# Kernel optimization log

Measured on AMD Instinct MI355X. Metric: run time of the kernel, lower is better.

Reference implementation:

```python
import jax, jax.numpy as jnp
import numpy as np

B, T, C = 4, 4096, 1024
H = 16
NBLOCKS, BSIZE = 32, 128
HD = C // H  # 64


def setup_inputs() -> dict:
    key = jax.random.key(0)
    ks = jax.random.split(key, 8)
    s = 1.0 / np.sqrt(C)
    return {
        "x": jax.random.normal(ks[0], (B, T, C), dtype=jnp.float32),
        "Wq": jax.random.uniform(ks[1], (C, C), jnp.float32, -s, s),
        "bq": jax.random.uniform(ks[2], (C,), jnp.float32, -s, s),
        "Wk": jax.random.uniform(ks[3], (C, C), jnp.float32, -s, s),
        "Wv": jax.random.uniform(ks[4], (C, C), jnp.float32, -s, s),
        "bv": jax.random.uniform(ks[5], (C,), jnp.float32, -s, s),
        "Wo": jax.random.uniform(ks[6], (C, C), jnp.float32, -s, s),
        "bo": jax.random.uniform(ks[7], (C,), jnp.float32, -s, s),
    }


def reference(x, Wq, bq, Wk, Wv, bv, Wo, bo):
    # Linear projections (torch F.linear: x @ W.T + b; key has no bias)
    q = x @ Wq.T + bq
    k = x @ Wk.T
    v = x @ Wv.T + bv

    scale = HD ** (-0.25)
    # reshape to (B, nblocks, bsize, H, head_dim); scale applied to q and k
    q = q.reshape(B, NBLOCKS, BSIZE, H, HD) * scale
    k = k.reshape(B, NBLOCKS, BSIZE, H, HD) * scale
    v = v.reshape(B, NBLOCKS, BSIZE, H, HD)

    # block-local scores: (B, H, nblocks, bsize, bsize)
    qk = jnp.einsum('bnqhd,bnkhd->bhnqk', q, k)
    w = jax.nn.softmax(qk.astype(jnp.float32), axis=-1).astype(q.dtype)
    # attention output: (B, H, nblocks, bsize, head_dim)
    o = jnp.einsum('bhnqk,bnkhd->bhnqd', w, v)
    # -> (B, nblocks, bsize, H, head_dim) -> (B, T, C)
    o = o.transpose(0, 2, 3, 1, 4).reshape(B, T, C)
    return o @ Wo.T + bo
```

## Files before the change

### kernel.cpp

```cpp
#include <hip/hip_runtime.h>
#include <stdint.h>

#define Bb   4
#define Tt   4096
#define Cc   1024
#define Hh   16
#define HDd  64
#define NBn  32
#define BSs  128
#define MTOT (Bb*Tt)

typedef short s16;
typedef __attribute__((ext_vector_type(8))) short  short8;
typedef __attribute__((ext_vector_type(4))) float  f32x4;
typedef __attribute__((ext_vector_type(4))) int    int4v;

__device__ __forceinline__ s16 f2bf(float f) {
  union { float f; uint32_t u; } c; c.f = f;
  return (s16)((c.u + 0x7fffu + ((c.u >> 16) & 1u)) >> 16);
}

typedef const __attribute__((address_space(1))) void* gas_p;
typedef __attribute__((address_space(3))) void*       las_p;
__device__ __forceinline__ void lds16(const void* g, void* l) {
  __builtin_amdgcn_global_load_lds((gas_p)g, (las_p)l, 16, 0, 0);
}

__global__ __launch_bounds__(256) void cvt_x(const float* __restrict__ in, s16* __restrict__ out) {
  int i = blockIdx.x * 256 + threadIdx.x;
  const f32x4* p = (const f32x4*)(in + (size_t)i * 8);
  f32x4 a = p[0], b = p[1];
  short8 o;
  o[0]=f2bf(a[0]); o[1]=f2bf(a[1]); o[2]=f2bf(a[2]); o[3]=f2bf(a[3]);
  o[4]=f2bf(b[0]); o[5]=f2bf(b[1]); o[6]=f2bf(b[2]); o[7]=f2bf(b[3]);
  *(short8*)(out + (size_t)i * 8) = o;
}

__global__ __launch_bounds__(256) void cvt_w(const float* w0, const float* w1,
                                             const float* w2, const float* w3,
                                             s16* o0, s16* o1, s16* o2, s16* o3) {
  int i = blockIdx.x * 256 + threadIdx.x;
  int which = i >> 17;
  int j = i & 131071;
  const float* w = which == 0 ? w0 : which == 1 ? w1 : which == 2 ? w2 : w3;
  s16*         o = which == 0 ? o0 : which == 1 ? o1 : which == 2 ? o2 : o3;
  const f32x4* p = (const f32x4*)(w + (size_t)j * 8);
  f32x4 a = p[0], b = p[1];
  short8 v;
  v[0]=f2bf(a[0]); v[1]=f2bf(a[1]); v[2]=f2bf(a[2]); v[3]=f2bf(a[3]);
  v[4]=f2bf(b[0]); v[5]=f2bf(b[1]); v[6]=f2bf(b[2]); v[7]=f2bf(b[3]);
  *(short8*)(o + (size_t)j * 8) = v;
}

template <bool OUT_BF16, int NXT>
__global__ __launch_bounds__(512, 2) void gemm256(const s16* __restrict__ Ag, const s16* __restrict__ Bg,
                                                  const float* b0, const float* b1, const float* b2,
                                                  void* o0, void* o1, void* o2) {
  __shared__ s16 smem[65536];

  const int tid = threadIdx.x;
  const int w = tid >> 6, l = tid & 63;
  const int lr = l & 15, lk = l >> 4;
  const int wm = w >> 2, wn = w & 3;

  const int lid = blockIdx.x;
  const int xcd = lid & 7, s0 = lid >> 3;
  const int my = xcd * 8 + s0 / NXT;
  const int nx = s0 - (s0 / NXT) * NXT;
  const int mBase = my * 256, nBase = nx * 256;

  f32x4 acc[8][4];
#pragma unroll
  for (int i = 0; i < 8; ++i)
#pragma unroll
    for (int j = 0; j < 4; ++j) acc[i][j] = (f32x4){0.f, 0.f, 0.f, 0.f};

  auto stage_tile = [&](int slot, int k0) {
    s16* Asl = smem + slot * 16384;
    s16* Bsl = smem + 32768 + slot * 16384;
#pragma unroll
    for (int L = 0; L < 4; ++L) {
      int s = L * 512 + tid;
      int r = s >> 3;
      int kg = (s & 7) ^ (r & 7);
      int wbase = (L * 512 + (tid & ~63)) * 8;
      lds16(Ag + (size_t)(mBase + r) * Cc + (k0 + kg * 8), Asl + wbase);
      lds16(Bg + (size_t)(nBase + r) * Cc + (k0 + kg * 8), Bsl + wbase);
    }
  };

  stage_tile(0, 0);
  __syncthreads();

  for (int kt = 0; kt < 16; ++kt) {
    const int c = kt & 1;
    const s16* Asc = smem + c * 16384;
    const s16* Bsc = smem + 32768 + c * 16384;

    if (kt < 15) stage_tile(c ^ 1, (kt + 1) * 64);

    short8 bk[4][2];
#pragma unroll
    for (int nt = 0; nt < 4; ++nt)
#pragma unroll
      for (int kk = 0; kk < 2; ++kk) {
        int row = wn * 64 + nt * 16 + lr;
        bk[nt][kk] = *(const short8*)&Bsc[row * 64 + (((kk * 4 + lk) ^ (lr & 7)) * 8)];
      }

#pragma unroll
    for (int q = 0; q < 4; ++q) {
      short8 af[2][2];
#pragma unroll
      for (int mt2 = 0; mt2 < 2; ++mt2)
#pragma unroll
        for (int kk = 0; kk < 2; ++kk) {
          int row = wm * 128 + (q * 2 + mt2) * 16 + lr;
          af[mt2][kk] = *(const short8*)&Asc[row * 64 + (((kk * 4 + lk) ^ (lr & 7)) * 8)];
        }
      __builtin_amdgcn_s_setprio(1);
#pragma unroll
      for (int mt2 = 0; mt2 < 2; ++mt2)
#pragma unroll
        for (int nt = 0; nt < 4; ++nt)
#pragma unroll
          for (int kk = 0; kk < 2; ++kk)
            acc[q * 2 + mt2][nt] = __builtin_amdgcn_mfma_f32_16x16x32_bf16(
                af[mt2][kk], bk[nt][kk], acc[q * 2 + mt2][nt], 0, 0, 0);
      __builtin_amdgcn_s_setprio(0);
      if (q == 3) asm volatile("s_waitcnt vmcnt(0)" ::: "memory");
      __builtin_amdgcn_sched_barrier(0);
      asm volatile("s_barrier" ::: "memory");
      __builtin_amdgcn_sched_barrier(0);
    }
  }

  if (OUT_BF16) {
    const int seg = nBase >> 10;
    const float* bias = seg == 0 ? b0 : (seg == 1 ? b1 : b2);
    s16* outp = (s16*)(seg == 0 ? o0 : (seg == 1 ? o1 : o2));
    const int colL = nBase & 1023;
    s16* Cs = smem;
#pragma unroll
    for (int h = 0; h < 2; ++h) {
      if (wm == h) {
#pragma unroll
        for (int nt = 0; nt < 4; ++nt) {
          int col = wn * 64 + nt * 16 + lr;
          float bb = bias ? bias[colL + col] : 0.0f;
#pragma unroll
          for (int mt = 0; mt < 8; ++mt) {
            int r0 = mt * 16 + lk * 4;
#pragma unroll
            for (int i = 0; i < 4; ++i)
              Cs[(r0 + i) * 264 + col] = f2bf(acc[mt][nt][i] + bb);
          }
        }
      }
      __syncthreads();
#pragma unroll
      for (int t = 0; t < 8; ++t) {
        int s2 = t * 512 + tid;
        int r = s2 >> 5, g = s2 & 31;
        *(short8*)&outp[(size_t)(mBase + h * 128 + r) * 1024 + colL + g * 8] =
            *(const short8*)&Cs[r * 264 + g * 8];
      }
      __syncthreads();
    }
  } else {
    float* outp = (float*)o0;
#pragma unroll
    for (int nt = 0; nt < 4; ++nt) {
      int col = nBase + wn * 64 + nt * 16 + lr;
      float bb = b0[col];
#pragma unroll
      for (int mt = 0; mt < 8; ++mt) {
        int row0 = mBase + wm * 128 + mt * 16 + lk * 4;
#pragma unroll
        for (int i = 0; i < 4; ++i)
          outp[(size_t)(row0 + i) * 1024 + col] = acc[mt][nt][i] + bb;
      }
    }
  }
}

__global__ __launch_bounds__(256) void attn_kernel(const s16* __restrict__ Q, const s16* __restrict__ K,
                                                   const s16* __restrict__ V, s16* __restrict__ O) {
  __shared__ s16   u_qkp[19456];
  __shared__ s16   vsT[64 * 136];
  __shared__ float invSum[128];

  const int tid = threadIdx.x;
  const int w = tid >> 6, l = tid & 63;
  const int lr = l & 15, lk = l >> 4;
  const int bid = blockIdx.x;
  const int b = bid >> 9;
  const int n = (bid >> 4) & 31;
  const int h = bid & 15;
  const size_t tokBase = (size_t)b * Tt + (size_t)n * BSs;
  const int colBase = h * HDd;

  s16* qs = u_qkp;
  s16* ks = u_qkp + 9216;
  s16* P  = u_qkp;

#pragma unroll
  for (int t = 0; t < 4; ++t) {
    int s = t * 256 + tid;
    int r = s >> 3, g = s & 7;
    size_t gidx = (tokBase + r) * Cc + colBase + g * 8;
    int4v  dq = *(const int4v*)&Q[gidx];
    int4v  dk = *(const int4v*)&K[gidx];
    short8 dv = *(const short8*)&V[gidx];
    *(int4v*)&qs[r * 72 + g * 8] = dq;
    *(int4v*)&ks[r * 72 + g * 8] = dk;
    int rg = r >> 3, rl = r & 7;
#pragma unroll
    for (int e = 0; e < 8; ++e) {
      int d = g * 8 + e;
      vsT[d * 136 + ((rg ^ e ^ g) << 3) + rl] = dv[e];
    }
  }
  __syncthreads();

  f32x4 accS[2][8];
#pragma unroll
  for (int mt = 0; mt < 2; ++mt)
#pragma unroll
    for (int nt = 0; nt < 8; ++nt) accS[mt][nt] = (f32x4){0.f, 0.f, 0.f, 0.f};

#pragma unroll
  for (int st = 0; st < 2; ++st) {
    short8 aq[2], bk[8];
#pragma unroll
    for (int mt = 0; mt < 2; ++mt)
      aq[mt] = *(const short8*)&qs[(w * 32 + mt * 16 + lr) * 72 + st * 32 + lk * 8];
#pragma unroll
    for (int nt = 0; nt < 8; ++nt)
      bk[nt] = *(const short8*)&ks[(nt * 16 + lr) * 72 + st * 32 + lk * 8];
#pragma unroll
    for (int mt = 0; mt < 2; ++mt)
#pragma unroll
      for (int nt = 0; nt < 8; ++nt)
        accS[mt][nt] = __builtin_amdgcn_mfma_f32_16x16x32_bf16(aq[mt], bk[nt], accS[mt][nt], 0, 0, 0);
  }

#pragma unroll
  for (int mt = 0; mt < 2; ++mt)
#pragma unroll
    for (int i = 0; i < 4; ++i) {
      float m = accS[mt][0][i];
#pragma unroll
      for (int nt = 1; nt < 8; ++nt) m = fmaxf(m, accS[mt][nt][i]);
      m = fmaxf(m, __shfl_xor(m, 1));
      m = fmaxf(m, __shfl_xor(m, 2));
      m = fmaxf(m, __shfl_xor(m, 4));
      m = fmaxf(m, __shfl_xor(m, 8));
      float sum = 0.f;
#pragma unroll
      for (int nt = 0; nt < 8; ++nt) {
        float p = __expf((accS[mt][nt][i] - m) * 0.125f);
        sum += p;
        accS[mt][nt][i] = p;
      }
      sum += __shfl_xor(sum, 1);
      sum += __shfl_xor(sum, 2);
      sum += __shfl_xor(sum, 4);
      sum += __shfl_xor(sum, 8);
      if (lr == 0) invSum[w * 32 + mt * 16 + lk * 4 + i] = 1.0f / sum;
    }
  __syncthreads();

#pragma unroll
  for (int mt = 0; mt < 2; ++mt)
#pragma unroll
    for (int nt = 0; nt < 8; ++nt)
#pragma unroll
      for (int i = 0; i < 4; ++i)
        P[(w * 32 + mt * 16 + lk * 4 + i) * 152 + nt * 16 + lr] = f2bf(accS[mt][nt][i]);
  __syncthreads();

  f32x4 accO[2][4];
#pragma unroll
  for (int mt = 0; mt < 2; ++mt)
#pragma unroll
    for (int nt = 0; nt < 4; ++nt) accO[mt][nt] = (f32x4){0.f, 0.f, 0.f, 0.f};

#pragma unroll
  for (int st = 0; st < 4; ++st) {
    short8 ap[2], bv[4];
#pragma unroll
    for (int mt = 0; mt < 2; ++mt)
      ap[mt] = *(const short8*)&P[(w * 32 + mt * 16 + lr) * 152 + st * 32 + lk * 8];
#pragma unroll
    for (int nt = 0; nt < 4; ++nt) {
      int d = nt * 16 + lr;
      bv[nt] = *(const short8*)&vsT[d * 136 + ((((st * 4 + lk) ^ (d & 7) ^ (d >> 3))) << 3)];
    }
#pragma unroll
    for (int mt = 0; mt < 2; ++mt)
#pragma unroll
      for (int nt = 0; nt < 4; ++nt)
        accO[mt][nt] = __builtin_amdgcn_mfma_f32_16x16x32_bf16(ap[mt], bv[nt], accO[mt][nt], 0, 0, 0);
  }

#pragma unroll
  for (int mt = 0; mt < 2; ++mt)
#pragma unroll
    for (int nt = 0; nt < 4; ++nt)
#pragma unroll
      for (int i = 0; i < 4; ++i) {
        int rl = w * 32 + mt * 16 + lk * 4 + i;
        int d = nt * 16 + lr;
        float v = accO[mt][nt][i] * invSum[rl];
        O[(tokBase + rl) * Cc + colBase + d] = f2bf(v);
      }
}

extern "C" void kernel_launch(void* const* d_in, const int* in_sizes, int n_in,
                              void* d_out, int out_size, void* d_ws, size_t ws_size,
                              hipStream_t stream) {
  const float* x  = (const float*)d_in[0];
  const float* Wq = (const float*)d_in[1];
  const float* bq = (const float*)d_in[2];
  const float* Wk = (const float*)d_in[3];
  const float* Wv = (const float*)d_in[4];
  const float* bv = (const float*)d_in[5];
  const float* Wo = (const float*)d_in[6];
  const float* bo = (const float*)d_in[7];

  if (ws_size < (size_t)75497472) return;
  char* ws = (char*)d_ws;
  s16* xb  = (s16*)(ws);
  s16* wqb = (s16*)(ws + 33554432);
  s16* wkb = (s16*)(ws + 35651584);
  s16* wvb = (s16*)(ws + 37748736);
  s16* wob = (s16*)(ws + 39845888);
  s16* Qb  = (s16*)(ws + 41943040);
  s16* Kb  = (s16*)((char*)d_out);
  s16* Vb  = (s16*)((char*)d_out + 33554432);

  cvt_x<<<8192, 256, 0, stream>>>(x, xb);
  cvt_w<<<2048, 256, 0, stream>>>(Wq, Wk, Wv, Wo, wqb, wkb, wvb, wob);

  gemm256<true, 12><<<8 * 8 * 12, 512, 0, stream>>>(xb, wqb, bq, nullptr, bv, Qb, Kb, Vb);

  attn_kernel<<<Bb * NBn * Hh, 256, 0, stream>>>(Qb, Kb, Vb, Qb);

  gemm256<false, 4><<<8 * 8 * 4, 512, 0, stream>>>(Qb, wob, bo, bo, bo, (float*)d_out, nullptr, nullptr);
}
```

Before: 317.0 us.

## Interleave next-tile global-to-LDS staging across GEMM sub-phases with partial waits

Breaks the per-k-tile staging of the A and B tiles into four half-tile chunks, issuing one chunk per compute sub-phase instead of all at the start of the iteration. Partial vmcnt waits (vmcnt(4), vmcnt(1)) replace the full drain, and barriers are placed before and after each MFMA group. The aim is to spread memory traffic across the iteration and keep some loads in flight across barriers. In exchange, correctness now depends on precise vmcnt accounting, and the extra barriers per sub-phase add synchronization cost.

```diff
diff --git a/kernel.cpp b/kernel.cpp
--- a/kernel.cpp
+++ b/kernel.cpp
@@ -75,49 +75,59 @@
 #pragma unroll
     for (int j = 0; j < 4; ++j) acc[i][j] = (f32x4){0.f, 0.f, 0.f, 0.f};
 
-  auto stage_tile = [&](int slot, int k0) {
-    s16* Asl = smem + slot * 16384;
-    s16* Bsl = smem + 32768 + slot * 16384;
-#pragma unroll
-    for (int L = 0; L < 4; ++L) {
-      int s = L * 512 + tid;
+  auto stage_half = [&](int slot, int k0, int h) {
+    const bool isA = (h >= 2);
+    const int rbase = (h & 1) << 7;
+    const s16* src = isA ? Ag : Bg;
+    const int gB = (isA ? mBase : nBase) + rbase;
+    s16* dsth = smem + (isA ? 0 : 32768) + slot * 16384 + rbase * 64;
+#pragma unroll
+    for (int j = 0; j < 2; ++j) {
+      int s = j * 512 + tid;
       int r = s >> 3;
       int kg = (s & 7) ^ (r & 7);
-      int wbase = (L * 512 + (tid & ~63)) * 8;
-      lds16(Ag + (size_t)(mBase + r) * Cc + (k0 + kg * 8), Asl + wbase);
-      lds16(Bg + (size_t)(nBase + r) * Cc + (k0 + kg * 8), Bsl + wbase);
+      lds16(src + (size_t)(gB + r) * Cc + (k0 + kg * 8),
+            dsth + (j * 512 + (tid & ~63)) * 8);
     }
   };
 
-  stage_tile(0, 0);
+  stage_half(0, 0, 0); stage_half(0, 0, 1); stage_half(0, 0, 2); stage_half(0, 0, 3);
+  asm volatile("s_waitcnt vmcnt(1)" ::: "memory");
   __syncthreads();
 
   for (int kt = 0; kt < 16; ++kt) {
     const int c = kt & 1;
     const s16* Asc = smem + c * 16384;
     const s16* Bsc = smem + 32768 + c * 16384;
-
-    if (kt < 15) stage_tile(c ^ 1, (kt + 1) * 64);
-
     short8 bk[4][2];
 #pragma unroll
-    for (int nt = 0; nt < 4; ++nt)
-#pragma unroll
-      for (int kk = 0; kk < 2; ++kk) {
-        int row = wn * 64 + nt * 16 + lr;
-        bk[nt][kk] = *(const short8*)&Bsc[row * 64 + (((kk * 4 + lk) ^ (lr & 7)) * 8)];
-      }
-
-#pragma unroll
-    for (int q = 0; q < 4; ++q) {
+    for (int p = 0; p < 4; ++p) {
+      if (p == 0) {
+#pragma unroll
+        for (int nt = 0; nt < 4; ++nt)
+#pragma unroll
+          for (int kk = 0; kk < 2; ++kk) {
+            int row = wn * 64 + nt * 16 + lr;
+            bk[nt][kk] = *(const short8*)&Bsc[row * 64 + (((kk * 4 + lk) ^ (row & 7)) * 8)];
+          }
+      }
       short8 af[2][2];
 #pragma unroll
       for (int mt2 = 0; mt2 < 2; ++mt2)
 #pragma unroll
         for (int kk = 0; kk < 2; ++kk) {
-          int row = wm * 128 + (q * 2 + mt2) * 16 + lr;
-          af[mt2][kk] = *(const short8*)&Asc[row * 64 + (((kk * 4 + lk) ^ (lr & 7)) * 8)];
+          int row = wm * 128 + (p * 2 + mt2) * 16 + lr;
+          af[mt2][kk] = *(const short8*)&Asc[row * 64 + (((kk * 4 + lk) ^ (row & 7)) * 8)];
         }
+      if (kt < 15) stage_half(c ^ 1, (kt + 1) * 64, p);
+      if (p == 1) {
+        if (kt < 15) asm volatile("s_waitcnt vmcnt(4)" ::: "memory");
+        else         asm volatile("s_waitcnt vmcnt(0)" ::: "memory");
+      }
+      if (p == 3)    asm volatile("s_waitcnt vmcnt(1)" ::: "memory");
+      __builtin_amdgcn_s_barrier();
+      asm volatile("s_waitcnt lgkmcnt(0)" ::: "memory");
+      __builtin_amdgcn_sched_barrier(0);
       __builtin_amdgcn_s_setprio(1);
 #pragma unroll
       for (int mt2 = 0; mt2 < 2; ++mt2)
@@ -125,13 +135,10 @@
         for (int nt = 0; nt < 4; ++nt)
 #pragma unroll
           for (int kk = 0; kk < 2; ++kk)
-            acc[q * 2 + mt2][nt] = __builtin_amdgcn_mfma_f32_16x16x32_bf16(
-                af[mt2][kk], bk[nt][kk], acc[q * 2 + mt2][nt], 0, 0, 0);
+            acc[p * 2 + mt2][nt] = __builtin_amdgcn_mfma_f32_16x16x32_bf16(
+                af[mt2][kk], bk[nt][kk], acc[p * 2 + mt2][nt], 0, 0, 0);
       __builtin_amdgcn_s_setprio(0);
-      if (q == 3) asm volatile("s_waitcnt vmcnt(0)" ::: "memory");
-      __builtin_amdgcn_sched_barrier(0);
-      asm volatile("s_barrier" ::: "memory");
-      __builtin_amdgcn_sched_barrier(0);
+      __builtin_amdgcn_s_barrier();
     }
   }
 
```

Result: no change. 320.6 us (+1.1%).

## Interleave split global-to-LDS prefetch with MFMA quads and cut barriers per k-tile

Applied to the files above, without the earlier changes.

The GEMM main loop now issues the next tile's B halves and A quarter-slices in stages, placed between the MFMA groups, instead of all at once at the start of the iteration. It uses partial vmcnt waits and two barriers per k-tile in place of four. A fragments are double-buffered so LDS reads for the next quad overlap the current MFMAs. The aim is to hide global load latency and reduce synchronisation stalls. In exchange the ordering is more fragile, since correctness depends on the vmcnt counts matching the exact load issue order.

```diff
diff --git a/kernel.cpp b/kernel.cpp
--- a/kernel.cpp
+++ b/kernel.cpp
@@ -75,67 +75,100 @@
 #pragma unroll
     for (int j = 0; j < 4; ++j) acc[i][j] = (f32x4){0.f, 0.f, 0.f, 0.f};
 
-  auto stage_tile = [&](int slot, int k0) {
-    s16* Asl = smem + slot * 16384;
-    s16* Bsl = smem + 32768 + slot * 16384;
-#pragma unroll
-    for (int L = 0; L < 4; ++L) {
-      int s = L * 512 + tid;
+  auto stage_pair = [&](s16* lbase, const s16* gbase, int gRowBase, int rowOff, int k0) {
+#pragma unroll
+    for (int j = 0; j < 2; ++j) {
+      int s = j * 512 + tid;
       int r = s >> 3;
       int kg = (s & 7) ^ (r & 7);
-      int wbase = (L * 512 + (tid & ~63)) * 8;
-      lds16(Ag + (size_t)(mBase + r) * Cc + (k0 + kg * 8), Asl + wbase);
-      lds16(Bg + (size_t)(nBase + r) * Cc + (k0 + kg * 8), Bsl + wbase);
+      lds16(gbase + (size_t)(gRowBase + rowOff + r) * Cc + (k0 + kg * 8),
+            lbase + rowOff * 64 + (j * 512 + (tid & ~63)) * 8);
     }
   };
-
-  stage_tile(0, 0);
-  __syncthreads();
+  auto stage_one = [&](s16* lbase, const s16* gbase, int gRowBase, int rowOff, int k0) {
+    int r = tid >> 3;
+    int kg = (tid & 7) ^ (r & 7);
+    lds16(gbase + (size_t)(gRowBase + rowOff + r) * Cc + (k0 + kg * 8),
+          lbase + rowOff * 64 + (tid & ~63) * 8);
+  };
+
+  auto rdquad = [&](short8 (&dst)[2][2], int q, const s16* Asrc) {
+#pragma unroll
+    for (int mt2 = 0; mt2 < 2; ++mt2)
+#pragma unroll
+      for (int kk = 0; kk < 2; ++kk) {
+        int row = wm * 128 + (q * 2 + mt2) * 16 + lr;
+        dst[mt2][kk] = *(const short8*)&Asrc[row * 64 + (((kk * 4 + lk) ^ (row & 7)) * 8)];
+      }
+  };
+  auto mfmaq = [&](int q, short8 (&src)[2][2], short8 (&bkk)[4][2]) {
+    __builtin_amdgcn_s_setprio(1);
+#pragma unroll
+    for (int mt2 = 0; mt2 < 2; ++mt2)
+#pragma unroll
+      for (int nt = 0; nt < 4; ++nt)
+#pragma unroll
+        for (int kk = 0; kk < 2; ++kk)
+          acc[q * 2 + mt2][nt] = __builtin_amdgcn_mfma_f32_16x16x32_bf16(
+              src[mt2][kk], bkk[nt][kk], acc[q * 2 + mt2][nt], 0, 0, 0);
+    __builtin_amdgcn_s_setprio(0);
+  };
+
+  {
+    s16* Asl = smem;
+    s16* Bsl = smem + 32768;
+    stage_pair(Bsl, Bg, nBase, 0, 0);
+    stage_pair(Bsl, Bg, nBase, 128, 0);
+    stage_one(Asl, Ag, mBase, 0, 0);
+    stage_one(Asl, Ag, mBase, 128, 0);
+    stage_one(Asl, Ag, mBase, 64, 0);
+    stage_one(Asl, Ag, mBase, 192, 0);
+  }
 
   for (int kt = 0; kt < 16; ++kt) {
     const int c = kt & 1;
     const s16* Asc = smem + c * 16384;
     const s16* Bsc = smem + 32768 + c * 16384;
-
-    if (kt < 15) stage_tile(c ^ 1, (kt + 1) * 64);
-
+    s16* Asl = smem + (c ^ 1) * 16384;
+    s16* Bsl = smem + 32768 + (c ^ 1) * 16384;
+    const int k1 = (kt + 1) * 64;
+    const bool pf = (kt < 15);
+
+    asm volatile("s_waitcnt lgkmcnt(0)" ::: "memory");
+    asm volatile("s_waitcnt vmcnt(2)" ::: "memory");
+    __builtin_amdgcn_s_barrier();
+
+    if (pf) stage_pair(Bsl, Bg, nBase, 0, k1);
     short8 bk[4][2];
 #pragma unroll
     for (int nt = 0; nt < 4; ++nt)
 #pragma unroll
       for (int kk = 0; kk < 2; ++kk) {
         int row = wn * 64 + nt * 16 + lr;
-        bk[nt][kk] = *(const short8*)&Bsc[row * 64 + (((kk * 4 + lk) ^ (lr & 7)) * 8)];
-      }
-
-#pragma unroll
-    for (int q = 0; q < 4; ++q) {
-      short8 af[2][2];
-#pragma unroll
-      for (int mt2 = 0; mt2 < 2; ++mt2)
-#pragma unroll
-        for (int kk = 0; kk < 2; ++kk) {
-          int row = wm * 128 + (q * 2 + mt2) * 16 + lr;
-          af[mt2][kk] = *(const short8*)&Asc[row * 64 + (((kk * 4 + lk) ^ (lr & 7)) * 8)];
-        }
-      __builtin_amdgcn_s_setprio(1);
-#pragma unroll
-      for (int mt2 = 0; mt2 < 2; ++mt2)
-#pragma unroll
-        for (int nt = 0; nt < 4; ++nt)
-#pragma unroll
-          for (int kk = 0; kk < 2; ++kk)
-            acc[q * 2 + mt2][nt] = __builtin_amdgcn_mfma_f32_16x16x32_bf16(
-                af[mt2][kk], bk[nt][kk], acc[q * 2 + mt2][nt], 0, 0, 0);
-      __builtin_amdgcn_s_setprio(0);
-      if (q == 3) asm volatile("s_waitcnt vmcnt(0)" ::: "memory");
-      __builtin_amdgcn_sched_barrier(0);
-      asm volatile("s_barrier" ::: "memory");
-      __builtin_amdgcn_sched_barrier(0);
-    }
+        bk[nt][kk] = *(const short8*)&Bsc[row * 64 + (((kk * 4 + lk) ^ (row & 7)) * 8)];
+      }
+    short8 afA[2][2], afB[2][2];
+    rdquad(afA, 0, Asc);
+    rdquad(afB, 1, Asc);
+    mfmaq(0, afA, bk);
+
+    if (pf) stage_pair(Bsl, Bg, nBase, 128, k1);
+    mfmaq(1, afB, bk);
+
+    if (pf) asm volatile("s_waitcnt vmcnt(4)" ::: "memory");
+    else    asm volatile("s_waitcnt vmcnt(0)" ::: "memory");
+    __builtin_amdgcn_s_barrier();
+    if (pf) { stage_one(Asl, Ag, mBase, 0, k1); stage_one(Asl, Ag, mBase, 128, k1); }
+    rdquad(afA, 2, Asc);
+    rdquad(afB, 3, Asc);
+    mfmaq(2, afA, bk);
+
+    if (pf) { stage_one(Asl, Ag, mBase, 64, k1); stage_one(Asl, Ag, mBase, 192, k1); }
+    mfmaq(3, afB, bk);
   }
 
   if (OUT_BF16) {
+    __syncthreads();
     const int seg = nBase >> 10;
     const float* bias = seg == 0 ? b0 : (seg == 1 ? b1 : b2);
     s16* outp = (s16*)(seg == 0 ? o0 : (seg == 1 ? o1 : o2));
```

Result: faster. 302.3 us (-4.6%).
